# Kernel tuning notes

Measured on AMD Instinct MI355X. Metric: run time of the kernel, lower is better.

The kernel has to match this reference:

```python
import jax, jax.numpy as jnp
import numpy as np

HEADS = 8


def setup_inputs() -> dict:
    key = jax.random.key(0)
    k0, k1, k2, k3 = jax.random.split(key, 4)
    N, C_in, T = 4, 256, 2048
    C_kq, C_out = 512, 512
    x = jax.random.normal(k0, (N, C_in, T), dtype=jnp.float32)
    # Conv1d(kernel_size=1, bias=False) weights squeezed to (out, in)
    Wq = jax.random.normal(k1, (C_kq, C_in), dtype=jnp.float32) * 0.02
    Wk = jax.random.normal(k2, (C_kq, C_in), dtype=jnp.float32) * 0.02
    Wv = jax.random.normal(k3, (C_out, C_in), dtype=jnp.float32) * 0.02
    return {"x": x, "Wq": Wq, "Wk": Wk, "Wv": Wv}


def reference(x, Wq, Wk, Wv):
    N, C, T = x.shape
    H = HEADS
    C_kq = Wq.shape[0]
    C_out = Wv.shape[0]
    dk = C_kq // H
    dv = C_out // H
    # 1x1 conv == per-timestep linear projection
    q = jnp.einsum('oc,nct->not', Wq, x).reshape(N, H, dk, T)
    k = jnp.einsum('oc,nct->not', Wk, x).reshape(N, H, dk, T)
    v = jnp.einsum('oc,nct->not', Wv, x).reshape(N, H, dv, T)
    scale = 1.0 / np.sqrt(dk)
    # scores[n,h,tk,tq] = sum_d q[n,h,d,tq] * k[n,h,d,tk]
    scores = jnp.einsum('nhdq,nhdk->nhkq', q, k) * scale
    attn = jax.nn.softmax(scores, axis=2)  # softmax over key axis tk
    # out[n,h,d,tq] = sum_tk attn[n,h,tk,tq] * v[n,h,d,tk]
    out = jnp.einsum('nhkq,nhdk->nhdq', attn, v)
    return out.reshape(N, C_out, T)
```

## Files before the change

kernel.cpp:

```cpp
#include <hip/hip_runtime.h>
#include <stdint.h>

#define T_SEQ 2048
#define CIN 256
#define COUT 512
#define NHEAD 8
#define DH 64
#define LROW 72

typedef __bf16 bf16x8 __attribute__((ext_vector_type(8)));
typedef float f32x4 __attribute__((ext_vector_type(4)));
typedef float f32x16 __attribute__((ext_vector_type(16)));
typedef unsigned short u16x8 __attribute__((ext_vector_type(8)));
typedef unsigned u32x4 __attribute__((ext_vector_type(4)));

static __device__ __forceinline__ unsigned short bf16_rne(float f) {
  unsigned u = __builtin_bit_cast(unsigned, f);
  u += 0x7FFFu + ((u >> 16) & 1u);
  return (unsigned short)(u >> 16);
}

static __device__ __forceinline__ unsigned cvt_pk_bf16(float lo, float hi) {
  unsigned r;
  asm("v_cvt_pk_bf16_f32 %0, %1, %2" : "=v"(r) : "v"(lo), "v"(hi));
  return r;
}

static __device__ __forceinline__ void plswap(unsigned& a, unsigned& b) {
  auto rr = __builtin_amdgcn_permlane32_swap((int)a, (int)b, false, false);
  a = (unsigned)rr[0];
  b = (unsigned)rr[1];
}

static __device__ __forceinline__ bf16x8 ld_frag(const unsigned short* p) {
  u16x8 v = *(const u16x8*)p;
  return __builtin_bit_cast(bf16x8, v);
}

__global__ __launch_bounds__(256) void pack_w_k(const float* __restrict__ wq,
                                                const float* __restrict__ wk,
                                                const float* __restrict__ wv,
                                                unsigned short* __restrict__ wb) {
  int i = blockIdx.x * 256 + threadIdx.x;
  const float* src = (i < 131072) ? wq : (i < 262144) ? wk : wv;
  wb[i] = bf16_rne(src[i & 131071]);
}

__global__ __launch_bounds__(256) void pack_xT_k(const float* __restrict__ x,
                                                 unsigned short* __restrict__ xT) {
  __shared__ float tile[64][65];
  const int n = blockIdx.z, c0 = blockIdx.y * 64, t0 = blockIdx.x * 64;
  const int i = threadIdx.x;
  {
    const int cc = i >> 2, tch = (i & 3) * 16;
    const float* src = x + ((size_t)n * CIN + c0 + cc) * T_SEQ + t0 + tch;
    const float4* s4 = (const float4*)src;
#pragma unroll
    for (int q = 0; q < 4; ++q) {
      float4 v = s4[q];
      tile[cc][tch + q * 4 + 0] = v.x;
      tile[cc][tch + q * 4 + 1] = v.y;
      tile[cc][tch + q * 4 + 2] = v.z;
      tile[cc][tch + q * 4 + 3] = v.w;
    }
  }
  __syncthreads();
  {
    const int tt = i >> 2, cch = (i & 3) * 16;
    unsigned short* dst = xT + ((size_t)n * T_SEQ + t0 + tt) * CIN + c0 + cch;
    u16x8 w0, w1;
#pragma unroll
    for (int j = 0; j < 8; ++j) w0[j] = bf16_rne(tile[cch + j][tt]);
#pragma unroll
    for (int j = 0; j < 8; ++j) w1[j] = bf16_rne(tile[cch + 8 + j][tt]);
    *(u16x8*)dst = w0;
    *(u16x8*)(dst + 8) = w1;
  }
}

__global__ __launch_bounds__(256) void proj_k(const unsigned short* __restrict__ wb,
                                              const unsigned short* __restrict__ xT,
                                              unsigned short* __restrict__ qb,
                                              unsigned short* __restrict__ kb,
                                              unsigned short* __restrict__ vb) {
  const int z = blockIdx.z;
  const int n = z / 3, w = z % 3;
  const unsigned short* W = wb + (size_t)w * COUT * CIN;
  const unsigned short* X = xT + (size_t)n * T_SEQ * CIN;
  const int tid = threadIdx.x, wave = tid >> 6, lane = tid & 63;
  const int c = lane & 15, g = lane >> 4;
  const int o0 = blockIdx.x * 64;
  const int t0 = blockIdx.y * 128 + wave * 32;

  f32x4 acc[2][4];
  const f32x4 z4 = {0.f, 0.f, 0.f, 0.f};
#pragma unroll
  for (int mt = 0; mt < 2; ++mt)
#pragma unroll
    for (int no = 0; no < 4; ++no) acc[mt][no] = z4;

  for (int c0 = 0; c0 < CIN; c0 += 32) {
    bf16x8 a[2], b[4];
#pragma unroll
    for (int mt = 0; mt < 2; ++mt)
      a[mt] = ld_frag(X + (size_t)(t0 + mt * 16 + c) * CIN + c0 + g * 8);
#pragma unroll
    for (int no = 0; no < 4; ++no)
      b[no] = ld_frag(W + (size_t)(o0 + no * 16 + c) * CIN + c0 + g * 8);
#pragma unroll
    for (int mt = 0; mt < 2; ++mt)
#pragma unroll
      for (int no = 0; no < 4; ++no)
        acc[mt][no] = __builtin_amdgcn_mfma_f32_16x16x32_bf16(a[mt], b[no], acc[mt][no], 0, 0, 0);
  }

  unsigned short* dst = (w == 0) ? qb : (w == 1) ? kb : vb;
  const float scale = (w == 0) ? 0.18033688011112043f : 1.0f;
  const int h = o0 >> 6;
  const size_t base = ((size_t)(n * NHEAD + h)) * T_SEQ * DH;
#pragma unroll
  for (int mt = 0; mt < 2; ++mt)
#pragma unroll
    for (int no = 0; no < 4; ++no)
#pragma unroll
      for (int r = 0; r < 4; ++r) {
        const int t = t0 + mt * 16 + 4 * g + r;
        const int d = no * 16 + c;
        if (w == 2) {
          dst[base + (size_t)d * T_SEQ + t] = bf16_rne(acc[mt][no][r]);
        } else {
          dst[base + (size_t)t * DH + d] = bf16_rne(acc[mt][no][r] * scale);
        }
      }
}

__global__ __launch_bounds__(256) void attn_k(const unsigned short* __restrict__ qb,
                                              const unsigned short* __restrict__ kb,
                                              const unsigned short* __restrict__ vbt,
                                              float* __restrict__ outp) {
  __shared__ unsigned short Kl[2][64 * LROW];
  __shared__ unsigned short Vt[2][64 * LROW];

  const int bid = blockIdx.x;
  const int sid = (bid & 7) * 64 + (bid >> 3);
  const int tqt = sid & 15, nh = sid >> 4;

  const int tid = threadIdx.x;
  const int wave = tid >> 6, lane = tid & 63;
  const int ln = lane & 31, hi = lane >> 5;
  const int tq0 = tqt * 128 + wave * 32;
  const unsigned short* Q = qb + (size_t)nh * T_SEQ * DH;
  const unsigned short* K = kb + (size_t)nh * T_SEQ * DH;
  const unsigned short* V = vbt + (size_t)nh * T_SEQ * DH;

  bf16x8 qf[4];
#pragma unroll
  for (int dblk = 0; dblk < 4; ++dblk)
    qf[dblk] = ld_frag(Q + (size_t)(tq0 + ln) * DH + dblk * 16 + hi * 8);

  const f32x16 z16 = {0.f, 0.f, 0.f, 0.f, 0.f, 0.f, 0.f, 0.f,
                      0.f, 0.f, 0.f, 0.f, 0.f, 0.f, 0.f, 0.f};
  f32x16 oacc0 = z16, oacc1 = z16;
  float l_run = 0.f;

  const int srow = tid & 63, sseg = tid >> 6;
  const unsigned short* kseg = K + (size_t)srow * DH + sseg * 16;
  const unsigned short* vseg = V + (size_t)srow * T_SEQ + sseg * 16;
  const int swoff = srow * LROW + sseg * 16;
  const int row0 = ln * LROW;
  const int row1 = (32 + ln) * LROW;
  const int hioff = hi * 8;

  unsigned short* krb = &Kl[0][0];
  unsigned short* kab = &Kl[1][0];
  unsigned short* vrb = &Vt[0][0];
  unsigned short* vab = &Vt[1][0];
  {
    u16x8 k0 = *(const u16x8*)kseg;
    u16x8 k1 = *(const u16x8*)(kseg + 8);
    u16x8 v0 = *(const u16x8*)vseg;
    u16x8 v1 = *(const u16x8*)(vseg + 8);
    *(u16x8*)&krb[swoff] = k0;
    *(u16x8*)&krb[swoff + 8] = k1;
    *(u16x8*)&vrb[swoff] = v0;
    *(u16x8*)&vrb[swoff + 8] = v1;
  }
  __syncthreads();

  const int NT = T_SEQ / 64;
  for (int t = 0; t < NT; ++t) {
    const bool pre = (t + 1 < NT);
    u16x8 kn0, kn1, vn0, vn1;
    if (pre) {
      const unsigned short* ks = kseg + (size_t)(t + 1) * (64 * DH);
      kn0 = *(const u16x8*)ks;
      kn1 = *(const u16x8*)(ks + 8);
      const unsigned short* vs = vseg + (size_t)(t + 1) * 64;
      vn0 = *(const u16x8*)vs;
      vn1 = *(const u16x8*)(vs + 8);
    }
    f32x16 sa0 = z16, sa1 = z16;
    __builtin_amdgcn_s_setprio(1);
#pragma unroll
    for (int dblk = 0; dblk < 4; ++dblk) {
      bf16x8 ka0 = ld_frag(krb + row0 + dblk * 16 + hioff);
      bf16x8 ka1 = ld_frag(krb + row1 + dblk * 16 + hioff);
      sa0 = __builtin_amdgcn_mfma_f32_32x32x16_bf16(ka0, qf[dblk], sa0, 0, 0, 0);
      sa1 = __builtin_amdgcn_mfma_f32_32x32x16_bf16(ka1, qf[dblk], sa1, 0, 0, 0);
    }
    __builtin_amdgcn_s_setprio(0);
    float p0[16], p1[16];
    float cs = 0.f;
#pragma unroll
    for (int r = 0; r < 16; ++r) {
      p0[r] = __builtin_amdgcn_exp2f(sa0[r]);
      p1[r] = __builtin_amdgcn_exp2f(sa1[r]);
      cs += p0[r] + p1[r];
    }
    cs += __shfl_xor(cs, 32);
    l_run += cs;
    unsigned W0[8], W1[8];
#pragma unroll
    for (int j = 0; j < 8; ++j) {
      W0[j] = cvt_pk_bf16(p0[2 * j], p0[2 * j + 1]);
      W1[j] = cvt_pk_bf16(p1[2 * j], p1[2 * j + 1]);
    }
    plswap(W0[0], W0[2]);
    plswap(W0[1], W0[3]);
    plswap(W0[4], W0[6]);
    plswap(W0[5], W0[7]);
    plswap(W1[0], W1[2]);
    plswap(W1[1], W1[3]);
    plswap(W1[4], W1[6]);
    plswap(W1[5], W1[7]);
    bf16x8 pa[4];
    {
      u32x4 f;
      f[0] = W0[0]; f[1] = W0[1]; f[2] = W0[2]; f[3] = W0[3];
      pa[0] = __builtin_bit_cast(bf16x8, f);
      f[0] = W0[4]; f[1] = W0[5]; f[2] = W0[6]; f[3] = W0[7];
      pa[1] = __builtin_bit_cast(bf16x8, f);
      f[0] = W1[0]; f[1] = W1[1]; f[2] = W1[2]; f[3] = W1[3];
      pa[2] = __builtin_bit_cast(bf16x8, f);
      f[0] = W1[4]; f[1] = W1[5]; f[2] = W1[6]; f[3] = W1[7];
      pa[3] = __builtin_bit_cast(bf16x8, f);
    }
    __builtin_amdgcn_s_setprio(1);
#pragma unroll
    for (int kbk = 0; kbk < 4; ++kbk) {
      bf16x8 vf0 = ld_frag(vrb + row0 + kbk * 16 + hioff);
      bf16x8 vf1 = ld_frag(vrb + row1 + kbk * 16 + hioff);
      oacc0 = __builtin_amdgcn_mfma_f32_32x32x16_bf16(pa[kbk], vf0, oacc0, 0, 0, 0);
      oacc1 = __builtin_amdgcn_mfma_f32_32x32x16_bf16(pa[kbk], vf1, oacc1, 0, 0, 0);
    }
    __builtin_amdgcn_s_setprio(0);
    if (pre) {
      *(u16x8*)&kab[swoff] = kn0;
      *(u16x8*)&kab[swoff + 8] = kn1;
      *(u16x8*)&vab[swoff] = vn0;
      *(u16x8*)&vab[swoff + 8] = vn1;
    }
    __syncthreads();
    unsigned short* tp;
    tp = krb; krb = kab; kab = tp;
    tp = vrb; vrb = vab; vab = tp;
  }

  float* lshare = (float*)&Kl[0][0];
  lshare[wave * 32 + ln] = l_run;
  __syncthreads();
  const int n = nh >> 3, h = nh & 7;
  const size_t obase = (size_t)(n * COUT + h * DH) * T_SEQ;
  const int d0 = ln, d1 = 32 + ln;
#pragma unroll
  for (int rq = 0; rq < 4; ++rq) {
    const int tbase = tq0 + 8 * rq + 4 * hi;
    f32x4 il = *(f32x4*)&lshare[wave * 32 + 8 * rq + 4 * hi];
    f32x4 o0, o1;
#pragma unroll
    for (int j = 0; j < 4; ++j) {
      const float inv = __builtin_amdgcn_rcpf(il[j]);
      o0[j] = oacc0[4 * rq + j] * inv;
      o1[j] = oacc1[4 * rq + j] * inv;
    }
    *(f32x4*)&outp[obase + (size_t)d0 * T_SEQ + tbase] = o0;
    *(f32x4*)&outp[obase + (size_t)d1 * T_SEQ + tbase] = o1;
  }
}

extern "C" void kernel_launch(void* const* d_in, const int* in_sizes, int n_in,
                              void* d_out, int out_size, void* d_ws, size_t ws_size,
                              hipStream_t stream) {
  (void)in_sizes; (void)n_in; (void)out_size; (void)ws_size;
  const float* x  = (const float*)d_in[0];
  const float* Wq = (const float*)d_in[1];
  const float* Wk = (const float*)d_in[2];
  const float* Wv = (const float*)d_in[3];
  float* outp = (float*)d_out;

  char* ws = (char*)d_ws;
  unsigned short* wb = (unsigned short*)ws;
  unsigned short* xT = (unsigned short*)(ws + 786432);
  unsigned short* qb = (unsigned short*)(ws + 4980736);
  unsigned short* kb = qb + 4194304;
  unsigned short* vb = kb + 4194304;

  pack_w_k<<<1536, 256, 0, stream>>>(Wq, Wk, Wv, wb);
  pack_xT_k<<<dim3(32, 4, 4), 256, 0, stream>>>(x, xT);
  proj_k<<<dim3(8, 16, 12), 256, 0, stream>>>(wb, xT, qb, kb, vb);
  attn_k<<<512, 256, 0, stream>>>(qb, kb, vb, outp);
}
```

Before: 107.4 us.

## Load K/V MFMA fragments directly from global memory and stage V transpose through LDS

```diff
diff --git a/kernel.cpp b/kernel.cpp
--- a/kernel.cpp
+++ b/kernel.cpp
@@ -6,7 +6,6 @@
 #define COUT 512
 #define NHEAD 8
 #define DH 64
-#define LROW 72
 
 typedef __bf16 bf16x8 __attribute__((ext_vector_type(8)));
 typedef float f32x4 __attribute__((ext_vector_type(4)));
@@ -83,6 +82,7 @@
                                               unsigned short* __restrict__ qb,
                                               unsigned short* __restrict__ kb,
                                               unsigned short* __restrict__ vb) {
+  __shared__ unsigned short vt_lds[64][136];
   const int z = blockIdx.z;
   const int n = z / 3, w = z % 3;
   const unsigned short* W = wb + (size_t)w * COUT * CIN;
@@ -114,33 +114,48 @@
         acc[mt][no] = __builtin_amdgcn_mfma_f32_16x16x32_bf16(a[mt], b[no], acc[mt][no], 0, 0, 0);
   }
 
-  unsigned short* dst = (w == 0) ? qb : (w == 1) ? kb : vb;
-  const float scale = (w == 0) ? 0.18033688011112043f : 1.0f;
   const int h = o0 >> 6;
   const size_t base = ((size_t)(n * NHEAD + h)) * T_SEQ * DH;
-#pragma unroll
-  for (int mt = 0; mt < 2; ++mt)
-#pragma unroll
-    for (int no = 0; no < 4; ++no)
-#pragma unroll
-      for (int r = 0; r < 4; ++r) {
-        const int t = t0 + mt * 16 + 4 * g + r;
+  if (w == 2) {
+#pragma unroll
+    for (int mt = 0; mt < 2; ++mt)
+#pragma unroll
+      for (int no = 0; no < 4; ++no) {
         const int d = no * 16 + c;
-        if (w == 2) {
-          dst[base + (size_t)d * T_SEQ + t] = bf16_rne(acc[mt][no][r]);
-        } else {
+        const int lt = (wave * 32) + mt * 16 + 4 * g;
+#pragma unroll
+        for (int pr = 0; pr < 2; ++pr) {
+          const unsigned pw = (unsigned)bf16_rne(acc[mt][no][2 * pr]) |
+                              ((unsigned)bf16_rne(acc[mt][no][2 * pr + 1]) << 16);
+          *(unsigned*)&vt_lds[d][lt + 2 * pr] = pw;
+        }
+      }
+    __syncthreads();
+    const int row = tid >> 2, seg = tid & 3;
+    unsigned short* dst = vb + base + (size_t)row * T_SEQ + blockIdx.y * 128 + seg * 32;
+    const unsigned short* srcl = &vt_lds[row][seg * 32];
+#pragma unroll
+    for (int q = 0; q < 4; ++q) *(u16x8*)(dst + q * 8) = *(const u16x8*)(srcl + q * 8);
+  } else {
+    unsigned short* dst = (w == 0) ? qb : kb;
+    const float scale = (w == 0) ? 0.18033688011112043f : 1.0f;
+#pragma unroll
+    for (int mt = 0; mt < 2; ++mt)
+#pragma unroll
+      for (int no = 0; no < 4; ++no)
+#pragma unroll
+        for (int r = 0; r < 4; ++r) {
+          const int t = t0 + mt * 16 + 4 * g + r;
+          const int d = no * 16 + c;
           dst[base + (size_t)t * DH + d] = bf16_rne(acc[mt][no][r] * scale);
         }
-      }
+  }
 }
 
 __global__ __launch_bounds__(256) void attn_k(const unsigned short* __restrict__ qb,
                                               const unsigned short* __restrict__ kb,
                                               const unsigned short* __restrict__ vbt,
                                               float* __restrict__ outp) {
-  __shared__ unsigned short Kl[2][64 * LROW];
-  __shared__ unsigned short Vt[2][64 * LROW];
-
   const int bid = blockIdx.x;
   const int sid = (bid & 7) * 64 + (bid >> 3);
   const int tqt = sid & 15, nh = sid >> 4;
@@ -163,50 +178,30 @@
   f32x16 oacc0 = z16, oacc1 = z16;
   float l_run = 0.f;
 
-  const int srow = tid & 63, sseg = tid >> 6;
-  const unsigned short* kseg = K + (size_t)srow * DH + sseg * 16;
-  const unsigned short* vseg = V + (size_t)srow * T_SEQ + sseg * 16;
-  const int swoff = srow * LROW + sseg * 16;
-  const int row0 = ln * LROW;
-  const int row1 = (32 + ln) * LROW;
-  const int hioff = hi * 8;
-
-  unsigned short* krb = &Kl[0][0];
-  unsigned short* kab = &Kl[1][0];
-  unsigned short* vrb = &Vt[0][0];
-  unsigned short* vab = &Vt[1][0];
-  {
-    u16x8 k0 = *(const u16x8*)kseg;
-    u16x8 k1 = *(const u16x8*)(kseg + 8);
-    u16x8 v0 = *(const u16x8*)vseg;
-    u16x8 v1 = *(const u16x8*)(vseg + 8);
-    *(u16x8*)&krb[swoff] = k0;
-    *(u16x8*)&krb[swoff + 8] = k1;
-    *(u16x8*)&vrb[swoff] = v0;
-    *(u16x8*)&vrb[swoff + 8] = v1;
-  }
-  __syncthreads();
+  const unsigned short* kfb = K + (size_t)ln * DH + hi * 8;
+  const unsigned short* vfb = V + (size_t)ln * T_SEQ + hi * 8;
 
   const int NT = T_SEQ / 64;
   for (int t = 0; t < NT; ++t) {
-    const bool pre = (t + 1 < NT);
-    u16x8 kn0, kn1, vn0, vn1;
-    if (pre) {
-      const unsigned short* ks = kseg + (size_t)(t + 1) * (64 * DH);
-      kn0 = *(const u16x8*)ks;
-      kn1 = *(const u16x8*)(ks + 8);
-      const unsigned short* vs = vseg + (size_t)(t + 1) * 64;
-      vn0 = *(const u16x8*)vs;
-      vn1 = *(const u16x8*)(vs + 8);
+    const unsigned short* kt = kfb + (size_t)t * (64 * DH);
+    const unsigned short* vt = vfb + (size_t)t * 64;
+    bf16x8 ka0[4], ka1[4], vf0[4], vf1[4];
+#pragma unroll
+    for (int dblk = 0; dblk < 4; ++dblk) {
+      ka0[dblk] = ld_frag(kt + dblk * 16);
+      ka1[dblk] = ld_frag(kt + 32 * DH + dblk * 16);
+    }
+#pragma unroll
+    for (int kbk = 0; kbk < 4; ++kbk) {
+      vf0[kbk] = ld_frag(vt + kbk * 16);
+      vf1[kbk] = ld_frag(vt + 32 * T_SEQ + kbk * 16);
     }
     f32x16 sa0 = z16, sa1 = z16;
     __builtin_amdgcn_s_setprio(1);
 #pragma unroll
     for (int dblk = 0; dblk < 4; ++dblk) {
-      bf16x8 ka0 = ld_frag(krb + row0 + dblk * 16 + hioff);
-      bf16x8 ka1 = ld_frag(krb + row1 + dblk * 16 + hioff);
-      sa0 = __builtin_amdgcn_mfma_f32_32x32x16_bf16(ka0, qf[dblk], sa0, 0, 0, 0);
-      sa1 = __builtin_amdgcn_mfma_f32_32x32x16_bf16(ka1, qf[dblk], sa1, 0, 0, 0);
+      sa0 = __builtin_amdgcn_mfma_f32_32x32x16_bf16(ka0[dblk], qf[dblk], sa0, 0, 0, 0);
+      sa1 = __builtin_amdgcn_mfma_f32_32x32x16_bf16(ka1[dblk], qf[dblk], sa1, 0, 0, 0);
     }
     __builtin_amdgcn_s_setprio(0);
     float p0[16], p1[16];
@@ -248,38 +243,23 @@
     __builtin_amdgcn_s_setprio(1);
 #pragma unroll
     for (int kbk = 0; kbk < 4; ++kbk) {
-      bf16x8 vf0 = ld_frag(vrb + row0 + kbk * 16 + hioff);
-      bf16x8 vf1 = ld_frag(vrb + row1 + kbk * 16 + hioff);
-      oacc0 = __builtin_amdgcn_mfma_f32_32x32x16_bf16(pa[kbk], vf0, oacc0, 0, 0, 0);
-      oacc1 = __builtin_amdgcn_mfma_f32_32x32x16_bf16(pa[kbk], vf1, oacc1, 0, 0, 0);
+      oacc0 = __builtin_amdgcn_mfma_f32_32x32x16_bf16(pa[kbk], vf0[kbk], oacc0, 0, 0, 0);
+      oacc1 = __builtin_amdgcn_mfma_f32_32x32x16_bf16(pa[kbk], vf1[kbk], oacc1, 0, 0, 0);
     }
     __builtin_amdgcn_s_setprio(0);
-    if (pre) {
-      *(u16x8*)&kab[swoff] = kn0;
-      *(u16x8*)&kab[swoff + 8] = kn1;
-      *(u16x8*)&vab[swoff] = vn0;
-      *(u16x8*)&vab[swoff + 8] = vn1;
-    }
-    __syncthreads();
-    unsigned short* tp;
-    tp = krb; krb = kab; kab = tp;
-    tp = vrb; vrb = vab; vab = tp;
-  }
-
-  float* lshare = (float*)&Kl[0][0];
-  lshare[wave * 32 + ln] = l_run;
-  __syncthreads();
+  }
+
   const int n = nh >> 3, h = nh & 7;
   const size_t obase = (size_t)(n * COUT + h * DH) * T_SEQ;
   const int d0 = ln, d1 = 32 + ln;
 #pragma unroll
   for (int rq = 0; rq < 4; ++rq) {
     const int tbase = tq0 + 8 * rq + 4 * hi;
-    f32x4 il = *(f32x4*)&lshare[wave * 32 + 8 * rq + 4 * hi];
     f32x4 o0, o1;
 #pragma unroll
     for (int j = 0; j < 4; ++j) {
-      const float inv = __builtin_amdgcn_rcpf(il[j]);
+      const float lv = __shfl(l_run, 8 * rq + 4 * hi + j);
+      const float inv = __builtin_amdgcn_rcpf(lv);
       o0[j] = oacc0[4 * rq + j] * inv;
       o1[j] = oacc1[4 * rq + j] * inv;
     }
```

Measured after the change: 173.1 us. 61.2% more time.

## Split attention key range across two wave groups and stage V transpose via LDS

Applied to the files above, without the earlier changes.

```diff
diff --git a/kernel.cpp b/kernel.cpp
--- a/kernel.cpp
+++ b/kernel.cpp
@@ -83,6 +83,7 @@
                                               unsigned short* __restrict__ qb,
                                               unsigned short* __restrict__ kb,
                                               unsigned short* __restrict__ vb) {
+  __shared__ unsigned short vt_lds[64][136];
   const int z = blockIdx.z;
   const int n = z / 3, w = z % 3;
   const unsigned short* W = wb + (size_t)w * COUT * CIN;
@@ -114,32 +115,50 @@
         acc[mt][no] = __builtin_amdgcn_mfma_f32_16x16x32_bf16(a[mt], b[no], acc[mt][no], 0, 0, 0);
   }
 
-  unsigned short* dst = (w == 0) ? qb : (w == 1) ? kb : vb;
-  const float scale = (w == 0) ? 0.18033688011112043f : 1.0f;
   const int h = o0 >> 6;
   const size_t base = ((size_t)(n * NHEAD + h)) * T_SEQ * DH;
-#pragma unroll
-  for (int mt = 0; mt < 2; ++mt)
-#pragma unroll
-    for (int no = 0; no < 4; ++no)
-#pragma unroll
-      for (int r = 0; r < 4; ++r) {
-        const int t = t0 + mt * 16 + 4 * g + r;
+  if (w == 2) {
+#pragma unroll
+    for (int mt = 0; mt < 2; ++mt)
+#pragma unroll
+      for (int no = 0; no < 4; ++no) {
         const int d = no * 16 + c;
-        if (w == 2) {
-          dst[base + (size_t)d * T_SEQ + t] = bf16_rne(acc[mt][no][r]);
-        } else {
+        const int lt = (wave * 32) + mt * 16 + 4 * g;
+#pragma unroll
+        for (int pr = 0; pr < 2; ++pr) {
+          const unsigned pw = (unsigned)bf16_rne(acc[mt][no][2 * pr]) |
+                              ((unsigned)bf16_rne(acc[mt][no][2 * pr + 1]) << 16);
+          *(unsigned*)&vt_lds[d][lt + 2 * pr] = pw;
+        }
+      }
+    __syncthreads();
+    const int row = tid >> 2, seg = tid & 3;
+    unsigned short* dst = vb + base + (size_t)row * T_SEQ + blockIdx.y * 128 + seg * 32;
+    const unsigned short* srcl = &vt_lds[row][seg * 32];
+#pragma unroll
+    for (int q = 0; q < 4; ++q) *(u16x8*)(dst + q * 8) = *(const u16x8*)(srcl + q * 8);
+  } else {
+    unsigned short* dst = (w == 0) ? qb : kb;
+    const float scale = (w == 0) ? 0.18033688011112043f : 1.0f;
+#pragma unroll
+    for (int mt = 0; mt < 2; ++mt)
+#pragma unroll
+      for (int no = 0; no < 4; ++no)
+#pragma unroll
+        for (int r = 0; r < 4; ++r) {
+          const int t = t0 + mt * 16 + 4 * g + r;
+          const int d = no * 16 + c;
           dst[base + (size_t)t * DH + d] = bf16_rne(acc[mt][no][r] * scale);
         }
-      }
-}
-
-__global__ __launch_bounds__(256) void attn_k(const unsigned short* __restrict__ qb,
+  }
+}
+
+__global__ __launch_bounds__(512) void attn_k(const unsigned short* __restrict__ qb,
                                               const unsigned short* __restrict__ kb,
                                               const unsigned short* __restrict__ vbt,
                                               float* __restrict__ outp) {
-  __shared__ unsigned short Kl[2][64 * LROW];
-  __shared__ unsigned short Vt[2][64 * LROW];
+  __shared__ unsigned short Kl[2][2][64 * LROW];
+  __shared__ unsigned short Vt[2][2][64 * LROW];
 
   const int bid = blockIdx.x;
   const int sid = (bid & 7) * 64 + (bid >> 3);
@@ -147,8 +166,9 @@
 
   const int tid = threadIdx.x;
   const int wave = tid >> 6, lane = tid & 63;
+  const int half = wave >> 2;
   const int ln = lane & 31, hi = lane >> 5;
-  const int tq0 = tqt * 128 + wave * 32;
+  const int tq0 = tqt * 128 + (wave & 3) * 32;
   const unsigned short* Q = qb + (size_t)nh * T_SEQ * DH;
   const unsigned short* K = kb + (size_t)nh * T_SEQ * DH;
   const unsigned short* V = vbt + (size_t)nh * T_SEQ * DH;
@@ -163,18 +183,19 @@
   f32x16 oacc0 = z16, oacc1 = z16;
   float l_run = 0.f;
 
-  const int srow = tid & 63, sseg = tid >> 6;
-  const unsigned short* kseg = K + (size_t)srow * DH + sseg * 16;
-  const unsigned short* vseg = V + (size_t)srow * T_SEQ + sseg * 16;
+  const int ht = tid & 255;
+  const int srow = ht & 63, sseg = ht >> 6;
+  const unsigned short* kseg = K + (size_t)(half * 1024 + srow) * DH + sseg * 16;
+  const unsigned short* vseg = V + (size_t)srow * T_SEQ + half * 1024 + sseg * 16;
   const int swoff = srow * LROW + sseg * 16;
   const int row0 = ln * LROW;
   const int row1 = (32 + ln) * LROW;
   const int hioff = hi * 8;
 
-  unsigned short* krb = &Kl[0][0];
-  unsigned short* kab = &Kl[1][0];
-  unsigned short* vrb = &Vt[0][0];
-  unsigned short* vab = &Vt[1][0];
+  unsigned short* krb = &Kl[half][0][0];
+  unsigned short* kab = &Kl[half][1][0];
+  unsigned short* vrb = &Vt[half][0][0];
+  unsigned short* vab = &Vt[half][1][0];
   {
     u16x8 k0 = *(const u16x8*)kseg;
     u16x8 k1 = *(const u16x8*)(kseg + 8);
@@ -187,9 +208,9 @@
   }
   __syncthreads();
 
-  const int NT = T_SEQ / 64;
-  for (int t = 0; t < NT; ++t) {
-    const bool pre = (t + 1 < NT);
+  const int NT2 = T_SEQ / 64 / 2;
+  for (int t = 0; t < NT2; ++t) {
+    const bool pre = (t + 1 < NT2);
     u16x8 kn0, kn1, vn0, vn1;
     if (pre) {
       const unsigned short* ks = kseg + (size_t)(t + 1) * (64 * DH);
@@ -266,25 +287,42 @@
     tp = vrb; vrb = vab; vab = tp;
   }
 
-  float* lshare = (float*)&Kl[0][0];
-  lshare[wave * 32 + ln] = l_run;
+  float* mbuf = (float*)&Kl[0][0][0];
+  const int MS = 2112;
+  if (half == 1) {
+    float* mb = mbuf + (wave - 4) * MS;
+#pragma unroll
+    for (int r = 0; r < 16; ++r) mb[r * 64 + lane] = oacc0[r];
+#pragma unroll
+    for (int r = 0; r < 16; ++r) mb[1024 + r * 64 + lane] = oacc1[r];
+    mb[2048 + lane] = l_run;
+  }
   __syncthreads();
-  const int n = nh >> 3, h = nh & 7;
-  const size_t obase = (size_t)(n * COUT + h * DH) * T_SEQ;
-  const int d0 = ln, d1 = 32 + ln;
-#pragma unroll
-  for (int rq = 0; rq < 4; ++rq) {
-    const int tbase = tq0 + 8 * rq + 4 * hi;
-    f32x4 il = *(f32x4*)&lshare[wave * 32 + 8 * rq + 4 * hi];
-    f32x4 o0, o1;
-#pragma unroll
-    for (int j = 0; j < 4; ++j) {
-      const float inv = __builtin_amdgcn_rcpf(il[j]);
-      o0[j] = oacc0[4 * rq + j] * inv;
-      o1[j] = oacc1[4 * rq + j] * inv;
-    }
-    *(f32x4*)&outp[obase + (size_t)d0 * T_SEQ + tbase] = o0;
-    *(f32x4*)&outp[obase + (size_t)d1 * T_SEQ + tbase] = o1;
+  if (half == 0) {
+    float* mb = mbuf + wave * MS;
+#pragma unroll
+    for (int r = 0; r < 16; ++r) oacc0[r] += mb[r * 64 + lane];
+#pragma unroll
+    for (int r = 0; r < 16; ++r) oacc1[r] += mb[1024 + r * 64 + lane];
+    l_run += mb[2048 + lane];
+
+    const int n = nh >> 3, h = nh & 7;
+    const size_t obase = (size_t)(n * COUT + h * DH) * T_SEQ;
+    const int d0 = ln, d1 = 32 + ln;
+#pragma unroll
+    for (int rq = 0; rq < 4; ++rq) {
+      const int tbase = tq0 + 8 * rq + 4 * hi;
+      f32x4 o0, o1;
+#pragma unroll
+      for (int j = 0; j < 4; ++j) {
+        const float lv = __shfl(l_run, 8 * rq + 4 * hi + j);
+        const float inv = __builtin_amdgcn_rcpf(lv);
+        o0[j] = oacc0[4 * rq + j] * inv;
+        o1[j] = oacc1[4 * rq + j] * inv;
+      }
+      *(f32x4*)&outp[obase + (size_t)d0 * T_SEQ + tbase] = o0;
+      *(f32x4*)&outp[obase + (size_t)d1 * T_SEQ + tbase] = o1;
+    }
   }
 }
 
@@ -308,5 +346,5 @@
   pack_w_k<<<1536, 256, 0, stream>>>(Wq, Wk, Wv, wb);
   pack_xT_k<<<dim3(32, 4, 4), 256, 0, stream>>>(x, xT);
   proj_k<<<dim3(8, 16, 12), 256, 0, stream>>>(wb, xT, qb, kb, vb);
-  attn_k<<<512, 256, 0, stream>>>(qb, kb, vb, outp);
-}
+  attn_k<<<512, 512, 0, stream>>>(qb, kb, vb, outp);
+}
```

Measured after the change: 105.5 us. No clear change (-1.7%).
